# Performance work log

Hardware: AMD Instinct MI355X
Metric: run time of the kernel (lower is better)

Reference implementation:

```python
import jax, jax.numpy as jnp
import numpy as np

FRAME = 160      # frame_size
K = 15           # frames_per_payload
ORDER = 12       # lpc_order
B = 4096
T = K * FRAME    # 2400


def setup_inputs() -> dict:
    key = jax.random.key(0)
    k1, k2 = jax.random.split(key)
    bits = jax.random.randint(k1, (B, K), 0, 2, dtype=jnp.int32)
    pcm = jax.random.uniform(k2, (B, T, 1), jnp.float32, minval=-1.0, maxval=1.0)
    alpha = jnp.float32(0.05)  # layer weight 'alpha' (alpha_init=0.05)
    return {"bits": bits, "pcm": pcm, "alpha": alpha}


def lpc_burg(x, order):
    """librosa.lpc (Burg's method), vectorized over all frames. x: (N, L)."""
    a = jnp.zeros((x.shape[0], order + 1), x.dtype).at[:, 0].set(1.0)
    f = x[:, 1:]          # forward prediction error
    b = x[:, :-1]         # backward prediction error
    den = jnp.sum(f * f + b * b, axis=-1)
    for i in range(order):  # small fixed-order unrolled loop
        reflect = -2.0 * jnp.sum(b * f, axis=-1) / den   # (N,)
        r = reflect[:, None]
        # a[j] <- a[j] + reflect * a[i+1-j] for j=0..i+1 (j=0 is a no-op since a[i+1]=0)
        a = a.at[:, : i + 2].set(a[:, : i + 2] + r * a[:, : i + 2][:, ::-1])
        f_tmp = f
        f = f + r * b
        b = b + r * f_tmp
        den = (1.0 - reflect * reflect) * den - b[:, -1] ** 2 - f[:, 0] ** 2
        f = f[:, 1:]
        b = b[:, :-1]
    return a  # (N, order+1), a[:,0]==1


def fir_filter(a, x):
    """scipy.signal.lfilter(a, [1.0], x): out[n] = sum_k a[k]*x[n-k], zero init."""
    L = x.shape[1]
    xpad = jnp.pad(x, ((0, 0), (ORDER, 0)))
    # X[:, n, k] = x[:, n-k]
    X = jnp.stack([xpad[:, ORDER - k: ORDER - k + L] for k in range(ORDER + 1)], axis=-1)
    return jnp.einsum('nlk,nk->nl', X, a)


def residual(pcm):
    # pcm: (B, T, 1) -> per-frame LPC residual, same shape
    frames = pcm[..., 0].reshape(-1, FRAME)                 # (B*K, FRAME)
    win = jnp.asarray(np.hanning(FRAME), dtype=pcm.dtype)   # Hann window for LPC analysis only
    a = lpc_burg(frames * win, ORDER)
    res = fir_filter(a, frames)                              # filter the RAW frame
    return res.reshape(pcm.shape[0], T, 1)


def reference(bits, pcm, alpha):
    res = residual(pcm)
    signs = 2.0 * bits.astype(pcm.dtype) - 1.0              # (B, K) in {-1,+1}
    chips = jnp.repeat(signs, FRAME, axis=1)[..., None]     # (B, T, 1)
    return pcm + alpha * res * chips
```

## Files before the change

kernel.cpp:

```cpp
#include <hip/hip_runtime.h>

#define FRAME 160
#define ORDER 12
#define NFRAMES (4096 * 15)
#define EPL 10
#define ROWP 174

typedef float v2f __attribute__((ext_vector_type(2)));

__device__ __forceinline__ v2f pkfma(v2f a, v2f b, v2f c) {
    return __builtin_elementwise_fma(a, b, c);
}
__device__ __forceinline__ v2f splat2(float v) { v2f r; r.x = v; r.y = v; return r; }

template<int CTRL>
__device__ __forceinline__ float dppf(float v) {
    return __int_as_float(__builtin_amdgcn_update_dpp(
        0, __float_as_int(v), CTRL, 0xF, 0xF, true));
}

__device__ __forceinline__ float rowsum16(float v) {
    v += dppf<0xB1>(v);
    v += dppf<0x4E>(v);
    v += dppf<0x140>(v);
    v += dppf<0x141>(v);
    return v;
}
__device__ __forceinline__ v2f rowsum16v(v2f v) {
    v2f r; r.x = rowsum16(v.x); r.y = rowsum16(v.y); return r;
}

__global__ __launch_bounds__(256) void ResidualEmbedding_70798240907390_kernel(
    const int* __restrict__ bits, const float* __restrict__ pcm,
    const float* __restrict__ alpha_p, float* __restrict__ out)
{
    const int tid  = threadIdx.x;
    const int wave = tid >> 6;
    const int lane = tid & 63;
    const int g    = lane >> 4;
    const int s    = lane & 15;
    const int wf0  = (blockIdx.x * 4 + wave) * 8;
    const int fA   = wf0 + 2 * g;
    const int fB   = fA + 1;

    __shared__ __align__(16) v2f s_x[4][4][ROWP];
    __shared__ float s_win[161];
    __shared__ v2f  s_a[4][4][16];

    if (tid < 161) {
        float w = (tid < 160)
            ? 0.5f - 0.5f * __cosf(6.2831853071795864769f / 159.0f * (float)tid)
            : 0.0f;
        s_win[tid] = w;
    }
    if (lane < 48) { int gr = lane / 12, j = lane % 12; s_x[wave][gr][j] = splat2(0.f); }
    if (lane < 4)  s_x[wave][lane][172] = splat2(0.f);

    {
        const float* pAg = pcm + (size_t)fA * FRAME;
        const float* pBg = pcm + (size_t)fB * FRAME;
#pragma unroll
        for (int c = 0; c < 3; ++c) {
            int p = 4 * s + 64 * c;
            if (p < FRAME) {
                float4 a4 = *(const float4*)(pAg + p);
                float4 b4 = *(const float4*)(pBg + p);
                float4* dst = (float4*)&s_x[wave][g][12 + p];
                dst[0] = make_float4(a4.x, b4.x, a4.y, b4.y);
                dst[1] = make_float4(a4.z, b4.z, a4.w, b4.w);
            }
        }
    }
    __syncthreads();

    const v2f* X = &s_x[wave][g][12];
    const int p0 = s * EPL;

    v2f F[EPL], B[EPL];
    {
        v2f pr[EPL + 1];
#pragma unroll
        for (int j = 0; j <= EPL; ++j)
            pr[j] = X[p0 + j] * s_win[p0 + j];
#pragma unroll
        for (int t = 0; t < EPL; ++t) { F[t] = pr[t + 1]; B[t] = pr[t]; }
    }
    if (s == 15) B[EPL - 1] = splat2(0.f);
    v2f dpF = splat2(0.f), dpB = splat2(0.f);
#pragma unroll
    for (int t = 0; t < EPL; ++t) {
        dpF = pkfma(F[t], F[t], dpF);
        dpB = pkfma(B[t], B[t], dpB);
    }
    v2f den = rowsum16v(dpF + dpB);

    v2f a  = (s == 0) ? splat2(1.f) : splat2(0.f);
    v2f ar = (s == 1) ? splat2(1.f) : splat2(0.f);
    v2f cp = splat2(0.f), dsc = splat2(0.f);

#pragma unroll
    for (int i = 0; i < ORDER; ++i) {
        v2f q0 = splat2(0.f), q1 = splat2(0.f);
#pragma unroll
        for (int t = 0; t < EPL; t += 2) {
            q0 = pkfma(F[t],     B[t],     q0);
            q1 = pkfma(F[t + 1], B[t + 1], q1);
        }
        v2f num = rowsum16v(q0 + q1);
        if (i > 0) den = dsc - rowsum16v(cp);
        v2f r;
        r.x = -2.0f * num.x * __builtin_amdgcn_rcpf(den.x);
        r.y = -2.0f * num.y * __builtin_amdgcn_rcpf(den.y);

        v2f an  = pkfma(r, ar, a);
        v2f arn = pkfma(r, a, ar);
        a = an;
        ar.x = dppf<0x111>(arn.x);
        ar.y = dppf<0x111>(arn.y);

#pragma unroll
        for (int t = 0; t < EPL; ++t) {
            v2f fo = F[t];
            F[t] = pkfma(r, B[t], fo);
            B[t] = pkfma(r, fo, B[t]);
        }

        const int pe = 158 - i;
        const int SL = pe / EPL, SS = pe % EPL;
        v2f fe = (s == 0)  ? F[0]  : splat2(0.f);
        v2f be = (s == SL) ? B[SS] : splat2(0.f);
        cp  = pkfma(fe, fe, be * be);
        dsc = pkfma(-(r * r), den, den);

        v2f up;
        up.x = dppf<0x101>(F[0].x);
        up.y = dppf<0x101>(F[0].y);
#pragma unroll
        for (int t = 0; t < EPL - 1; ++t) F[t] = F[t + 1];
        F[EPL - 1] = up;
        if (s == SL) B[SS] = splat2(0.f);
    }

    s_a[wave][g][s] = a;
    __syncthreads();
    v2f ak[ORDER + 1];
#pragma unroll
    for (int k = 0; k <= ORDER; ++k) ak[k] = s_a[wave][g][k];

    v2f Xw[EPL + ORDER];
#pragma unroll
    for (int j = 0; j < EPL + ORDER; ++j) Xw[j] = X[p0 - ORDER + j];

    const float alpha = alpha_p[0];
    v2f ac;
    ac.x = alpha * (2.0f * (float)bits[fA] - 1.0f);
    ac.y = alpha * (2.0f * (float)bits[fB] - 1.0f);

    float* oA = out + (size_t)fA * FRAME + p0;
    float* oB = out + (size_t)fB * FRAME + p0;
#pragma unroll
    for (int t = 0; t < EPL; t += 2) {
        v2f acc0 = splat2(0.f), acc1 = splat2(0.f);
#pragma unroll
        for (int k = 0; k <= ORDER; ++k) {
            acc0 = pkfma(ak[k], Xw[ORDER + t - k],     acc0);
            acc1 = pkfma(ak[k], Xw[ORDER + t + 1 - k], acc1);
        }
        v2f r0 = pkfma(ac, acc0, Xw[ORDER + t]);
        v2f r1 = pkfma(ac, acc1, Xw[ORDER + t + 1]);
        *(float2*)(oA + t) = make_float2(r0.x, r1.x);
        *(float2*)(oB + t) = make_float2(r0.y, r1.y);
    }
}

extern "C" void kernel_launch(void* const* d_in, const int* in_sizes, int n_in,
                              void* d_out, int out_size, void* d_ws, size_t ws_size,
                              hipStream_t stream) {
    const int*   bits  = (const int*)d_in[0];
    const float* pcm   = (const float*)d_in[1];
    const float* alpha = (const float*)d_in[2];
    float*       out   = (float*)d_out;

    dim3 grid(NFRAMES / 32), block(256);
    hipLaunchKernelGGL(ResidualEmbedding_70798240907390_kernel, grid, block, 0, stream,
                       bits, pcm, alpha, out);
}
```

Before: 105.0 us.

## Split fused Burg+FIR kernel into two kernels via workspace coefficients

Splits the single fused kernel into two launches. The first runs the Burg recursion and writes the LPC coefficients to workspace, and the second reloads pcm and the coefficients to apply the FIR and the chip modulation. The likely aim is lower register and LDS pressure per kernel, and so higher occupancy. The cost is a second read of pcm, an extra global round trip for the coefficients, and an additional launch.

```diff
diff --git a/kernel.cpp b/kernel.cpp
--- a/kernel.cpp
+++ b/kernel.cpp
@@ -4,6 +4,8 @@
 #define ORDER 12
 #define NFRAMES (4096 * 15)
 #define EPL 10
+#define ROWK1 162
+#define PADF 12
 #define ROWP 174
 
 typedef float v2f __attribute__((ext_vector_type(2)));
@@ -18,7 +20,6 @@
     return __int_as_float(__builtin_amdgcn_update_dpp(
         0, __float_as_int(v), CTRL, 0xF, 0xF, true));
 }
-
 __device__ __forceinline__ float rowsum16(float v) {
     v += dppf<0xB1>(v);
     v += dppf<0x4E>(v);
@@ -30,22 +31,19 @@
     v2f r; r.x = rowsum16(v.x); r.y = rowsum16(v.y); return r;
 }
 
-__global__ __launch_bounds__(256) void ResidualEmbedding_70798240907390_kernel(
-    const int* __restrict__ bits, const float* __restrict__ pcm,
-    const float* __restrict__ alpha_p, float* __restrict__ out)
+__global__ __launch_bounds__(256) void burg_k1(
+    const float* __restrict__ pcm, float* __restrict__ acoef)
 {
     const int tid  = threadIdx.x;
     const int wave = tid >> 6;
     const int lane = tid & 63;
     const int g    = lane >> 4;
     const int s    = lane & 15;
-    const int wf0  = (blockIdx.x * 4 + wave) * 8;
-    const int fA   = wf0 + 2 * g;
-    const int fB   = fA + 1;
-
-    __shared__ __align__(16) v2f s_x[4][4][ROWP];
+    const int Gid  = (blockIdx.x * 4 + wave) * 4 + g;
+    const int fA   = 2 * Gid, fB = fA + 1;
+
+    __shared__ __align__(16) v2f s_x[4][4][ROWK1];
     __shared__ float s_win[161];
-    __shared__ v2f  s_a[4][4][16];
 
     if (tid < 161) {
         float w = (tid < 160)
@@ -53,9 +51,7 @@
             : 0.0f;
         s_win[tid] = w;
     }
-    if (lane < 48) { int gr = lane / 12, j = lane % 12; s_x[wave][gr][j] = splat2(0.f); }
-    if (lane < 4)  s_x[wave][lane][172] = splat2(0.f);
-
+    if (lane < 4) s_x[wave][lane][160] = splat2(0.f);
     {
         const float* pAg = pcm + (size_t)fA * FRAME;
         const float* pBg = pcm + (size_t)fB * FRAME;
@@ -65,7 +61,7 @@
             if (p < FRAME) {
                 float4 a4 = *(const float4*)(pAg + p);
                 float4 b4 = *(const float4*)(pBg + p);
-                float4* dst = (float4*)&s_x[wave][g][12 + p];
+                float4* dst = (float4*)&s_x[wave][g][p];
                 dst[0] = make_float4(a4.x, b4.x, a4.y, b4.y);
                 dst[1] = make_float4(a4.z, b4.z, a4.w, b4.w);
             }
@@ -73,7 +69,7 @@
     }
     __syncthreads();
 
-    const v2f* X = &s_x[wave][g][12];
+    const v2f* X = &s_x[wave][g][0];
     const int p0 = s * EPL;
 
     v2f F[EPL], B[EPL];
@@ -141,8 +137,50 @@
         if (s == SL) B[SS] = splat2(0.f);
     }
 
-    s_a[wave][g][s] = a;
+    if (s < ORDER + 1)
+        *(v2f*)(acoef + 2 * ((size_t)Gid * (ORDER + 1) + s)) = a;
+}
+
+__global__ __launch_bounds__(256) void fir_k2(
+    const int* __restrict__ bits, const float* __restrict__ pcm,
+    const float* __restrict__ alpha_p, const float* __restrict__ acoef,
+    float* __restrict__ out)
+{
+    const int tid  = threadIdx.x;
+    const int wave = tid >> 6;
+    const int lane = tid & 63;
+    const int g    = lane >> 4;
+    const int s    = lane & 15;
+    const int Gid  = (blockIdx.x * 4 + wave) * 4 + g;
+    const int fA   = 2 * Gid, fB = fA + 1;
+
+    __shared__ __align__(16) v2f s_x[4][4][ROWP];
+    __shared__ v2f s_a[4][4][16];
+
+    if (s < ORDER + 1)
+        s_a[wave][g][s] = *(const v2f*)(acoef + 2 * ((size_t)Gid * (ORDER + 1) + s));
+    if (lane < 48) { int gr = lane / 12, j = lane % 12; s_x[wave][gr][j] = splat2(0.f); }
+    if (lane < 4)  s_x[wave][lane][PADF + FRAME] = splat2(0.f);
+    {
+        const float* pAg = pcm + (size_t)fA * FRAME;
+        const float* pBg = pcm + (size_t)fB * FRAME;
+#pragma unroll
+        for (int c = 0; c < 3; ++c) {
+            int p = 4 * s + 64 * c;
+            if (p < FRAME) {
+                float4 a4 = *(const float4*)(pAg + p);
+                float4 b4 = *(const float4*)(pBg + p);
+                float4* dst = (float4*)&s_x[wave][g][PADF + p];
+                dst[0] = make_float4(a4.x, b4.x, a4.y, b4.y);
+                dst[1] = make_float4(a4.z, b4.z, a4.w, b4.w);
+            }
+        }
+    }
     __syncthreads();
+
+    const v2f* X = &s_x[wave][g][PADF];
+    const int p0 = s * EPL;
+
     v2f ak[ORDER + 1];
 #pragma unroll
     for (int k = 0; k <= ORDER; ++k) ak[k] = s_a[wave][g][k];
@@ -180,8 +218,9 @@
     const float* pcm   = (const float*)d_in[1];
     const float* alpha = (const float*)d_in[2];
     float*       out   = (float*)d_out;
+    float*       acoef = (float*)d_ws;
 
     dim3 grid(NFRAMES / 32), block(256);
-    hipLaunchKernelGGL(ResidualEmbedding_70798240907390_kernel, grid, block, 0, stream,
-                       bits, pcm, alpha, out);
-}
+    hipLaunchKernelGGL(burg_k1, grid, block, 0, stream, pcm, acoef);
+    hipLaunchKernelGGL(fir_k2,  grid, block, 0, stream, bits, pcm, alpha, acoef, out);
+}
```

Measured after the change: 116.7 us. 11.2% more time.
